# Kernel optimization log

Hardware: AMD Instinct MI355X
Metric: run time of the kernel (lower is better)

The kernel has to match this reference:

```python
import jax, jax.numpy as jnp
import numpy as np

DEPTH = 8  # dilation_depth; dilation for layer i is 2**(i % DEPTH)


def causal_conv(x, w, b, dilation):
    # x: [B,C,T], w: [O,I,K] -> causal dilated conv, output [B,O,T]
    pad = (w.shape[-1] - 1) * dilation
    xp = jnp.pad(x, ((0, 0), (0, 0), (pad, 0)))
    y = jax.lax.conv_general_dilated(
        xp, w, window_strides=(1,), padding='VALID',
        rhs_dilation=(dilation,), dimension_numbers=('NCW', 'OIW', 'NCW'))
    return y + b[None, :, None]


def conv1x1(x, w, b):
    # x: [B,C,T], w: [O,C] -> [B,O,T]
    return jnp.einsum('oc,bct->bot', w, x) + b[None, :, None]


def setup_inputs() -> dict:
    key = jax.random.key(0)
    ks = jax.random.split(key, 20)
    B, T, F, E = 16, 2048, 32, 16
    R, S, O, NOUT, L = 256, 128, 64, 24, 32  # residual, skip, out_size, n_output, layers
    s = 0.05
    return {
        'X_batch': jax.random.normal(ks[0], (B, T, F), jnp.float32),
        'X_batch_ex': jax.random.normal(ks[1], (B, E), jnp.float32),
        'w_in': jax.random.normal(ks[2], (R, F, 2), jnp.float32) * s,
        'b_in': jax.random.normal(ks[3], (R,), jnp.float32) * s,
        'w_filter': jax.random.normal(ks[4], (L, R, R, 2), jnp.float32) * s,
        'b_filter': jax.random.normal(ks[5], (L, R), jnp.float32) * s,
        'w_gate': jax.random.normal(ks[6], (L, R, R, 2), jnp.float32) * s,
        'b_gate': jax.random.normal(ks[7], (L, R), jnp.float32) * s,
        'w_res': jax.random.normal(ks[8], (L, R, R), jnp.float32) * s,
        'b_res': jax.random.normal(ks[9], (L, R), jnp.float32) * s,
        'w_skip': jax.random.normal(ks[10], (L, S, R), jnp.float32) * s,
        'b_skip': jax.random.normal(ks[11], (L, S), jnp.float32) * s,
        'w_out1': jax.random.normal(ks[12], (O, S), jnp.float32) * s,
        'b_out1': jax.random.normal(ks[13], (O,), jnp.float32) * s,
        'w_out2': jax.random.normal(ks[14], (O, O), jnp.float32) * s,
        'b_out2': jax.random.normal(ks[15], (O,), jnp.float32) * s,
        'w_lin': jax.random.normal(ks[16], (NOUT, O + E), jnp.float32) * s,
        'b_lin': jax.random.normal(ks[17], (NOUT,), jnp.float32) * s,
    }


def reference(X_batch, X_batch_ex, w_in, b_in, w_filter, b_filter, w_gate, b_gate,
              w_res, b_res, w_skip, b_skip, w_out1, b_out1, w_out2, b_out2,
              w_lin, b_lin):
    # [B,T,F] -> [B,F,T]
    x = jnp.transpose(X_batch, (0, 2, 1))
    x = causal_conv(x, w_in, b_in, 1)
    L = w_filter.shape[0]
    skip_sum = jnp.zeros((x.shape[0], w_skip.shape[1], x.shape[2]), x.dtype)
    for i in range(L):
        d = 2 ** (i % DEPTH)
        f = jnp.tanh(causal_conv(x, w_filter[i], b_filter[i], d))
        g = jax.nn.sigmoid(causal_conv(x, w_gate[i], b_gate[i], d))
        fx = conv1x1(f * g, w_res[i], b_res[i])
        skip_sum = skip_sum + conv1x1(fx, w_skip[i], b_skip[i])
        x = fx + x
    out = jax.nn.relu(skip_sum)
    out = jax.nn.relu(conv1x1(out, w_out1, b_out1))
    out = conv1x1(out, w_out2, b_out2)          # [B,O,T]
    h = out[:, :, -1]                            # last timestep, [B,O]
    h = jnp.concatenate([h, X_batch_ex], axis=1)
    h = jax.nn.relu(h)
    return h @ w_lin.T + b_lin                   # [B, n_output]
```

## Files before the change

### kernel.cpp

```cpp
#include <hip/hip_runtime.h>
#include <cmath>

#define TBUF 1024
#define RCH  256

typedef __bf16 bf16x8 __attribute__((ext_vector_type(8)));
typedef float  f32x4  __attribute__((ext_vector_type(4)));

__device__ inline unsigned short f2bf(float f) {
  unsigned u = __builtin_bit_cast(unsigned, f);
  u += 0x7FFFu + ((u >> 16) & 1u);
  return (unsigned short)(u >> 16);
}

__global__ __launch_bounds__(256) void transform_fgb(
    const float* __restrict__ wf, const float* __restrict__ wg, unsigned short* __restrict__ Wb)
{
  int idx = blockIdx.x * 256 + threadIdx.x;
  int c  = idx & 255;
  int op = (idx >> 8) & 511;
  int i  = idx >> 17;
  int o  = op & 255;
  const float* src = (op < 256) ? wf : wg;
  const float2 v = *(const float2*)&src[(((size_t)i * 256 + o) * 256 + c) << 1];
  unsigned short* dst = Wb + ((size_t)i * 512 + op) * 512;
  dst[c]       = f2bf(v.y);
  dst[256 + c] = f2bf(v.x);
}

__global__ __launch_bounds__(256) void transform_resb(
    const float* __restrict__ wr, unsigned short* __restrict__ Wrb)
{
  int idx = blockIdx.x * 256 + threadIdx.x;
  float4 v = ((const float4*)wr)[idx];
  uint2 o;
  o.x = (unsigned)f2bf(v.x) | ((unsigned)f2bf(v.y) << 16);
  o.y = (unsigned)f2bf(v.z) | ((unsigned)f2bf(v.w) << 16);
  ((uint2*)Wrb)[idx] = o;
}

__global__ __launch_bounds__(256) void transform_skip(
    const float* __restrict__ wsk, float* __restrict__ wskT)
{
  int idx = blockIdx.x * 256 + threadIdx.x;
  int s = idx & 127;
  int c = (idx >> 7) & 255;
  int i = idx >> 15;
  wskT[idx] = wsk[(i * 128 + s) * 256 + c];
}

__global__ __launch_bounds__(256) void transform_w2(
    const float* __restrict__ w_in, float* __restrict__ w2)
{
  int idx = blockIdx.x * 256 + threadIdx.x;
  int r = idx & 255;
  int fk = idx >> 8;
  int f = fk & 31, k = fk >> 5;
  w2[idx] = w_in[r * 64 + f * 2 + k];
}

__global__ __launch_bounds__(256) void in_conv(
    const float* __restrict__ X, const float* __restrict__ w2,
    const float* __restrict__ b_in, float* __restrict__ xb,
    unsigned short* __restrict__ xbb)
{
  const int bid   = blockIdx.x;
  const int b     = bid & 15;
  const int chunk = bid >> 4;
  const int r     = threadIdx.x;
  __shared__ float Xs[17][32];
  const int tt0 = chunk << 4;
  const int t0  = tt0 + 1024;
  for (int idx = r; idx < 17 * 32; idx += 256) {
    int row = idx >> 5, f = idx & 31;
    Xs[row][f] = X[((size_t)b * 2048 + (t0 - 1 + row)) * 32 + f];
  }
  __syncthreads();
  float w0[32], w1[32];
  #pragma unroll
  for (int f = 0; f < 32; ++f) {
    w0[f] = w2[f * 256 + r];
    w1[f] = w2[(32 + f) * 256 + r];
  }
  const float bias = b_in[r];
  float4 prev[8], cur[8];
  #pragma unroll
  for (int q = 0; q < 8; ++q) prev[q] = *(const float4*)&Xs[0][q * 4];
  #pragma unroll
  for (int j = 0; j < 16; ++j) {
    #pragma unroll
    for (int q = 0; q < 8; ++q) cur[q] = *(const float4*)&Xs[j + 1][q * 4];
    float a = bias;
    #pragma unroll
    for (int q = 0; q < 8; ++q) {
      a = fmaf(w0[q*4+0], prev[q].x, a); a = fmaf(w1[q*4+0], cur[q].x, a);
      a = fmaf(w0[q*4+1], prev[q].y, a); a = fmaf(w1[q*4+1], cur[q].y, a);
      a = fmaf(w0[q*4+2], prev[q].z, a); a = fmaf(w1[q*4+2], cur[q].z, a);
      a = fmaf(w0[q*4+3], prev[q].w, a); a = fmaf(w1[q*4+3], cur[q].w, a);
    }
    int tt = tt0 + j;
    size_t off = ((size_t)b * TBUF + tt) * RCH + r;
    if (tt < 3) { xb[off] = 0.f; xbb[off] = 0; }
    else        { xb[off] = a;   xbb[off] = f2bf(a); }
    #pragma unroll
    for (int q = 0; q < 8; ++q) prev[q] = cur[q];
  }
}

__global__ __launch_bounds__(512, 4) void layer_fused(
    const unsigned short* __restrict__ xbb_r, float* __restrict__ xb,
    unsigned short* __restrict__ xbb_w,
    const unsigned short* __restrict__ Wb,
    const unsigned short* __restrict__ Wrb,
    const float* __restrict__ bF, const float* __restrict__ bG,
    const float* __restrict__ bR,
    int dd, int t_lo, float* __restrict__ fxs_i)
{
  __shared__ __align__(16) unsigned short As[64 * 520];
  const int bid  = blockIdx.x;
  const int b    = bid & 15;
  const int tile = bid >> 4;
  const int tid  = threadIdx.x;
  const int w    = tid >> 6;
  const int lane = tid & 63;
  const int l15  = lane & 15;
  const int lk8  = (lane >> 4) << 3;
  const int rr0  = (lane >> 4) << 2;
  const int tt0  = t_lo + tile * 64;
  const unsigned short* xB = xbb_r + ((size_t)b << 18);

  {
    const int c   = lane;
    const int tap = c >> 5;
    const int cg  = (c & 31) << 3;
    #pragma unroll
    for (int it = 0; it < 8; ++it) {
      int r = it * 8 + w;
      int tt = tt0 + r - tap * dd;
      tt = min(max(tt, 0), 1023);
      __builtin_amdgcn_global_load_lds(
          (const __attribute__((address_space(1))) unsigned int*)
              (xB + ((size_t)tt << 8) + cg),
          (__attribute__((address_space(3))) unsigned int*)
              ((char*)As + r * 1040),
          16, 0, 0);
    }
  }
  __syncthreads();

  f32x4 accf[4][2] = {};
  f32x4 accg[4][2] = {};
  const unsigned short* wf0 = Wb + (size_t)(32 * w + l15) * 512 + lk8;
  const unsigned short* wf1 = wf0 + (size_t)16 * 512;
  const unsigned short* wg0 = wf0 + (size_t)256 * 512;
  const unsigned short* wg1 = wf0 + (size_t)272 * 512;
  #pragma unroll 4
  for (int kc = 0; kc < 16; ++kc) {
    const int k0 = kc * 32;
    uint4 ubf0 = *(const uint4*)(wf0 + k0);
    uint4 ubf1 = *(const uint4*)(wf1 + k0);
    uint4 ubg0 = *(const uint4*)(wg0 + k0);
    uint4 ubg1 = *(const uint4*)(wg1 + k0);
    const int colb = (k0 + lk8) * 2;
    bf16x8 a[4];
    #pragma unroll
    for (int mf = 0; mf < 4; ++mf)
      a[mf] = *(const bf16x8*)((const char*)As + (mf * 16 + l15) * 1040 + colb);
    bf16x8 vf0 = __builtin_bit_cast(bf16x8, ubf0);
    bf16x8 vf1 = __builtin_bit_cast(bf16x8, ubf1);
    bf16x8 vg0 = __builtin_bit_cast(bf16x8, ubg0);
    bf16x8 vg1 = __builtin_bit_cast(bf16x8, ubg1);
    #pragma unroll
    for (int mf = 0; mf < 4; ++mf) {
      accf[mf][0] = __builtin_amdgcn_mfma_f32_16x16x32_bf16(a[mf], vf0, accf[mf][0], 0, 0, 0);
      accf[mf][1] = __builtin_amdgcn_mfma_f32_16x16x32_bf16(a[mf], vf1, accf[mf][1], 0, 0, 0);
      accg[mf][0] = __builtin_amdgcn_mfma_f32_16x16x32_bf16(a[mf], vg0, accg[mf][0], 0, 0, 0);
      accg[mf][1] = __builtin_amdgcn_mfma_f32_16x16x32_bf16(a[mf], vg1, accg[mf][1], 0, 0, 0);
    }
  }
  __syncthreads();

  unsigned short* Zs = As;
  const float bfv[2] = { bF[32 * w + l15], bF[32 * w + 16 + l15] };
  const float bgv[2] = { bG[32 * w + l15], bG[32 * w + 16 + l15] };
  #pragma unroll
  for (int mf = 0; mf < 4; ++mf)
    #pragma unroll
    for (int nf = 0; nf < 2; ++nf) {
      int col = 32 * w + nf * 16 + l15;
      #pragma unroll
      for (int j = 0; j < 4; ++j) {
        int row = mf * 16 + rr0 + j;
        float pf = accf[mf][nf][j] + bfv[nf];
        float pg = accg[mf][nf][j] + bgv[nf];
        float e2 = __expf(2.f * pf);
        float th = 1.f - 2.f / (e2 + 1.f);
        float sg = 1.f / (1.f + __expf(-pg));
        *(unsigned short*)((char*)Zs + row * 528 + col * 2) = f2bf(th * sg);
      }
    }
  __syncthreads();

  float* xBf = xb + ((size_t)b << 18);
  float xo_pre[4][4][2];
  #pragma unroll
  for (int mf = 0; mf < 4; ++mf)
    #pragma unroll
    for (int j = 0; j < 4; ++j) {
      int tt = min(tt0 + mf * 16 + rr0 + j, 1023);
      #pragma unroll
      for (int nf = 0; nf < 2; ++nf) {
        int o = 32 * w + nf * 16 + l15;
        xo_pre[mf][j][nf] = xBf[((size_t)tt << 8) + o];
      }
    }

  f32x4 acc[4][2] = {};
  const unsigned short* wr0 = Wrb + (size_t)(32 * w + l15) * 256 + lk8;
  const unsigned short* wr1 = wr0 + (size_t)16 * 256;
  #pragma unroll 4
  for (int kc = 0; kc < 8; ++kc) {
    uint4 ur0 = *(const uint4*)(wr0 + kc * 32);
    uint4 ur1 = *(const uint4*)(wr1 + kc * 32);
    const int colb = (kc * 32 + lk8) * 2;
    bf16x8 a[4];
    #pragma unroll
    for (int mf = 0; mf < 4; ++mf)
      a[mf] = *(const bf16x8*)((const char*)Zs + (mf * 16 + l15) * 528 + colb);
    bf16x8 v0 = __builtin_bit_cast(bf16x8, ur0);
    bf16x8 v1 = __builtin_bit_cast(bf16x8, ur1);
    #pragma unroll
    for (int mf = 0; mf < 4; ++mf) {
      acc[mf][0] = __builtin_amdgcn_mfma_f32_16x16x32_bf16(a[mf], v0, acc[mf][0], 0, 0, 0);
      acc[mf][1] = __builtin_amdgcn_mfma_f32_16x16x32_bf16(a[mf], v1, acc[mf][1], 0, 0, 0);
    }
  }

  const float brv[2] = { bR[32 * w + l15], bR[32 * w + 16 + l15] };
  unsigned short* xBb = xbb_w + ((size_t)b << 18);
  #pragma unroll
  for (int mf = 0; mf < 4; ++mf)
    #pragma unroll
    for (int j = 0; j < 4; ++j) {
      int tt = tt0 + mf * 16 + rr0 + j;
      if (tt > 1023) continue;
      #pragma unroll
      for (int nf = 0; nf < 2; ++nf) {
        int o = 32 * w + nf * 16 + l15;
        size_t off = ((size_t)tt << 8) + o;
        float fx = acc[mf][nf][j] + brv[nf];
        float xn = xo_pre[mf][j][nf] + fx;
        xBf[off] = xn;
        xBb[off] = f2bf(xn);
        if (tt == 1023) fxs_i[(size_t)b * 256 + o] = fx;
      }
    }
}

__global__ __launch_bounds__(128) void skip_partial(
    const float* __restrict__ fxs, const float* __restrict__ wskT,
    const float* __restrict__ b_skip, float* __restrict__ part)
{
  int i = blockIdx.x, b = blockIdx.y, s = threadIdx.x;
  __shared__ float fxsh[256];
  fxsh[s]       = fxs[((size_t)i * 16 + b) * 256 + s];
  fxsh[s + 128] = fxs[((size_t)i * 16 + b) * 256 + s + 128];
  __syncthreads();
  float a = b_skip[i * 128 + s];
  const float* wp = wskT + (size_t)i * 256 * 128 + s;
  #pragma unroll 4
  for (int c = 0; c < 256; c++)
    a = fmaf(wp[c * 128], fxsh[c], a);
  part[((size_t)i * 16 + b) * 128 + s] = a;
}

__global__ __launch_bounds__(128) void head2(
    const float* __restrict__ part, const float* __restrict__ w_o1,
    const float* __restrict__ b_o1, const float* __restrict__ w_o2,
    const float* __restrict__ b_o2, const float* __restrict__ w_lin,
    const float* __restrict__ b_lin, const float* __restrict__ Xex,
    float* __restrict__ out)
{
  int b = blockIdx.x, tid = threadIdx.x;
  __shared__ float sk[128];
  __shared__ float h1[64];
  __shared__ float hc[80];
  float a = 0.f;
  for (int i = 0; i < 32; i++) a += part[((size_t)i * 16 + b) * 128 + tid];
  sk[tid] = fmaxf(a, 0.f);
  __syncthreads();
  if (tid < 64) {
    float a1 = b_o1[tid];
    for (int s = 0; s < 128; s++) a1 = fmaf(w_o1[tid * 128 + s], sk[s], a1);
    h1[tid] = fmaxf(a1, 0.f);
  }
  __syncthreads();
  if (tid < 64) {
    float a2 = b_o2[tid];
    for (int j = 0; j < 64; j++) a2 = fmaf(w_o2[tid * 64 + j], h1[j], a2);
    hc[tid] = fmaxf(a2, 0.f);
  }
  if (tid >= 64 && tid < 80) hc[tid] = fmaxf(Xex[b * 16 + (tid - 64)], 0.f);
  __syncthreads();
  if (tid < 24) {
    float a3 = b_lin[tid];
    for (int j = 0; j < 80; j++) a3 = fmaf(w_lin[tid * 80 + j], hc[j], a3);
    out[b * 24 + tid] = a3;
  }
}

extern "C" void kernel_launch(void* const* d_in, const int* in_sizes, int n_in,
                              void* d_out, int out_size, void* d_ws, size_t ws_size,
                              hipStream_t stream)
{
  (void)in_sizes; (void)n_in; (void)out_size; (void)ws_size;
  const float* X     = (const float*)d_in[0];
  const float* Xex   = (const float*)d_in[1];
  const float* w_in  = (const float*)d_in[2];
  const float* b_in  = (const float*)d_in[3];
  const float* w_f   = (const float*)d_in[4];
  const float* b_f   = (const float*)d_in[5];
  const float* w_g   = (const float*)d_in[6];
  const float* b_g   = (const float*)d_in[7];
  const float* w_r   = (const float*)d_in[8];
  const float* b_r   = (const float*)d_in[9];
  const float* w_s   = (const float*)d_in[10];
  const float* b_s   = (const float*)d_in[11];
  const float* w_o1  = (const float*)d_in[12];
  const float* b_o1  = (const float*)d_in[13];
  const float* w_o2  = (const float*)d_in[14];
  const float* b_o2  = (const float*)d_in[15];
  const float* w_lin = (const float*)d_in[16];
  const float* b_lin = (const float*)d_in[17];

  float* ws   = (float*)d_ws;
  float* wskT = ws;
  float* xb   = wskT + 1048576;
  float* fxs  = xb   + 4194304;
  float* part = fxs  + 131072;
  float* w2   = part + 65536;
  unsigned short* Wb   = (unsigned short*)(w2 + 16384);
  unsigned short* Wrb  = Wb   + 8388608;
  unsigned short* xbbA = Wrb  + 2097152;
  unsigned short* xbbB = xbbA + 4194304;

  transform_fgb <<<16384, 256, 0, stream>>>(w_f, w_g, Wb);
  transform_resb<<<2048,  256, 0, stream>>>(w_r, Wrb);
  transform_skip<<<4096,  256, 0, stream>>>(w_s, wskT);
  transform_w2  <<<64,    256, 0, stream>>>(w_in, w2);
  in_conv<<<1024, 256, 0, stream>>>(X, w2, b_in, xb, xbbA);

  static const int wI[33] = {1021,1020,1018,1014,1006,990,958,894,
                             766,765,763,759,751,735,703,639,
                             511,510,508,504,496,480,448,384,
                             256,255,253,249,241,225,193,129,1};
  for (int i = 0; i < 32; i++) {
    int dd    = 1 << (i & 7);
    int Wout  = wI[i + 1];
    int t_lo  = TBUF - Wout;
    int tiles = (Wout + 63) / 64;
    unsigned short* xin  = (i & 1) ? xbbB : xbbA;
    unsigned short* xout = (i & 1) ? xbbA : xbbB;
    layer_fused<<<tiles * 16, 512, 0, stream>>>(
        xin, xb, xout,
        Wb + (size_t)i * 512 * 512, Wrb + (size_t)i * 256 * 256,
        b_f + i * 256, b_g + i * 256, b_r + i * 256,
        dd, t_lo, fxs + (size_t)i * 16 * 256);
  }
  skip_partial<<<dim3(32, 16), 128, 0, stream>>>(fxs, wskT, b_s, part);
  head2<<<16, 128, 0, stream>>>(part, w_o1, b_o1, w_o2, b_o2, w_lin, b_lin, Xex, (float*)d_out);
}
```

Measured before the change: 1.025 ms.

## Merge weight-prep kernels, prefetch residual weights early, relax layer occupancy bound

Folds the four weight-transform kernels into one launch with block-range dispatch, so three kernel launches are gone. In the fused layer kernel, the residual 1x1 weights are loaded into registers before the barrier and the gated activation, so their global latency overlaps other work. The launch-bounds minimum-blocks hint drops from 4 to 2 to leave room for the extra registers, which may lower occupancy.

```diff
diff --git a/kernel.cpp b/kernel.cpp
--- a/kernel.cpp
+++ b/kernel.cpp
@@ -13,50 +13,46 @@
   return (unsigned short)(u >> 16);
 }
 
-__global__ __launch_bounds__(256) void transform_fgb(
-    const float* __restrict__ wf, const float* __restrict__ wg, unsigned short* __restrict__ Wb)
-{
-  int idx = blockIdx.x * 256 + threadIdx.x;
-  int c  = idx & 255;
-  int op = (idx >> 8) & 511;
-  int i  = idx >> 17;
-  int o  = op & 255;
-  const float* src = (op < 256) ? wf : wg;
-  const float2 v = *(const float2*)&src[(((size_t)i * 256 + o) * 256 + c) << 1];
-  unsigned short* dst = Wb + ((size_t)i * 512 + op) * 512;
-  dst[c]       = f2bf(v.y);
-  dst[256 + c] = f2bf(v.x);
-}
-
-__global__ __launch_bounds__(256) void transform_resb(
-    const float* __restrict__ wr, unsigned short* __restrict__ Wrb)
-{
-  int idx = blockIdx.x * 256 + threadIdx.x;
-  float4 v = ((const float4*)wr)[idx];
-  uint2 o;
-  o.x = (unsigned)f2bf(v.x) | ((unsigned)f2bf(v.y) << 16);
-  o.y = (unsigned)f2bf(v.z) | ((unsigned)f2bf(v.w) << 16);
-  ((uint2*)Wrb)[idx] = o;
-}
-
-__global__ __launch_bounds__(256) void transform_skip(
-    const float* __restrict__ wsk, float* __restrict__ wskT)
-{
-  int idx = blockIdx.x * 256 + threadIdx.x;
-  int s = idx & 127;
-  int c = (idx >> 7) & 255;
-  int i = idx >> 15;
-  wskT[idx] = wsk[(i * 128 + s) * 256 + c];
-}
-
-__global__ __launch_bounds__(256) void transform_w2(
-    const float* __restrict__ w_in, float* __restrict__ w2)
-{
-  int idx = blockIdx.x * 256 + threadIdx.x;
-  int r = idx & 255;
-  int fk = idx >> 8;
-  int f = fk & 31, k = fk >> 5;
-  w2[idx] = w_in[r * 64 + f * 2 + k];
+__global__ __launch_bounds__(256) void prep(
+    const float* __restrict__ wf, const float* __restrict__ wg,
+    const float* __restrict__ wr, const float* __restrict__ wsk,
+    const float* __restrict__ w_in,
+    unsigned short* __restrict__ Wb, unsigned short* __restrict__ Wrb,
+    float* __restrict__ wskT, float* __restrict__ w2)
+{
+  const int bid = blockIdx.x;
+  const int tid = threadIdx.x;
+  if (bid < 16384) {
+    int idx = bid * 256 + tid;
+    int c  = idx & 255;
+    int op = (idx >> 8) & 511;
+    int i  = idx >> 17;
+    int o  = op & 255;
+    const float* src = (op < 256) ? wf : wg;
+    const float2 v = *(const float2*)&src[(((size_t)i * 256 + o) * 256 + c) << 1];
+    unsigned short* dst = Wb + ((size_t)i * 512 + op) * 512;
+    dst[c]       = f2bf(v.y);
+    dst[256 + c] = f2bf(v.x);
+  } else if (bid < 18432) {
+    int idx = (bid - 16384) * 256 + tid;
+    float4 v = ((const float4*)wr)[idx];
+    uint2 o;
+    o.x = (unsigned)f2bf(v.x) | ((unsigned)f2bf(v.y) << 16);
+    o.y = (unsigned)f2bf(v.z) | ((unsigned)f2bf(v.w) << 16);
+    ((uint2*)Wrb)[idx] = o;
+  } else if (bid < 22528) {
+    int idx = (bid - 18432) * 256 + tid;
+    int s = idx & 127;
+    int c = (idx >> 7) & 255;
+    int i = idx >> 15;
+    wskT[idx] = wsk[(i * 128 + s) * 256 + c];
+  } else {
+    int idx = (bid - 22528) * 256 + tid;
+    int r = idx & 255;
+    int fk = idx >> 8;
+    int f = fk & 31, k = fk >> 5;
+    w2[idx] = w_in[r * 64 + f * 2 + k];
+  }
 }
 
 __global__ __launch_bounds__(256) void in_conv(
@@ -107,7 +103,7 @@
   }
 }
 
-__global__ __launch_bounds__(512, 4) void layer_fused(
+__global__ __launch_bounds__(512, 2) void layer_fused(
     const unsigned short* __restrict__ xbb_r, float* __restrict__ xb,
     unsigned short* __restrict__ xbb_w,
     const unsigned short* __restrict__ Wb,
@@ -178,6 +174,15 @@
       accg[mf][1] = __builtin_amdgcn_mfma_f32_16x16x32_bf16(a[mf], vg1, accg[mf][1], 0, 0, 0);
     }
   }
+
+  const unsigned short* wr0 = Wrb + (size_t)(32 * w + l15) * 256 + lk8;
+  const unsigned short* wr1 = wr0 + (size_t)16 * 256;
+  uint4 urr[8][2];
+  #pragma unroll
+  for (int kc = 0; kc < 8; ++kc) {
+    urr[kc][0] = *(const uint4*)(wr0 + kc * 32);
+    urr[kc][1] = *(const uint4*)(wr1 + kc * 32);
+  }
   __syncthreads();
 
   unsigned short* Zs = As;
@@ -216,19 +221,15 @@
     }
 
   f32x4 acc[4][2] = {};
-  const unsigned short* wr0 = Wrb + (size_t)(32 * w + l15) * 256 + lk8;
-  const unsigned short* wr1 = wr0 + (size_t)16 * 256;
   #pragma unroll 4
   for (int kc = 0; kc < 8; ++kc) {
-    uint4 ur0 = *(const uint4*)(wr0 + kc * 32);
-    uint4 ur1 = *(const uint4*)(wr1 + kc * 32);
     const int colb = (kc * 32 + lk8) * 2;
     bf16x8 a[4];
     #pragma unroll
     for (int mf = 0; mf < 4; ++mf)
       a[mf] = *(const bf16x8*)((const char*)Zs + (mf * 16 + l15) * 528 + colb);
-    bf16x8 v0 = __builtin_bit_cast(bf16x8, ur0);
-    bf16x8 v1 = __builtin_bit_cast(bf16x8, ur1);
+    bf16x8 v0 = __builtin_bit_cast(bf16x8, urr[kc][0]);
+    bf16x8 v1 = __builtin_bit_cast(bf16x8, urr[kc][1]);
     #pragma unroll
     for (int mf = 0; mf < 4; ++mf) {
       acc[mf][0] = __builtin_amdgcn_mfma_f32_16x16x32_bf16(a[mf], v0, acc[mf][0], 0, 0, 0);
@@ -344,10 +345,7 @@
   unsigned short* xbbA = Wrb  + 2097152;
   unsigned short* xbbB = xbbA + 4194304;
 
-  transform_fgb <<<16384, 256, 0, stream>>>(w_f, w_g, Wb);
-  transform_resb<<<2048,  256, 0, stream>>>(w_r, Wrb);
-  transform_skip<<<4096,  256, 0, stream>>>(w_s, wskT);
-  transform_w2  <<<64,    256, 0, stream>>>(w_in, w2);
+  prep<<<22592, 256, 0, stream>>>(w_f, w_g, w_r, w_s, w_in, Wb, Wrb, wskT, w2);
   in_conv<<<1024, 256, 0, stream>>>(X, w2, b_in, xb, xbbA);
 
   static const int wI[33] = {1021,1020,1018,1014,1006,990,958,894,
```

Measured after the change: 1.268 ms. 23.7% more time.
